# Kernel tuning notes

Measured on AMD Instinct MI355X. Metric: run time of the kernel, lower is better.

Reference implementation:

```python
import jax, jax.numpy as jnp
import numpy as np

B, S, D = 4, 4096, 64
NEG = -1000000000.0

def setup_inputs() -> dict:
    key = jax.random.key(0)
    kq, kk, kv = jax.random.split(key, 3)
    Q = jax.random.normal(kq, (B, S, D), dtype=jnp.float32)
    K = jax.random.normal(kk, (B, S, D), dtype=jnp.float32)
    V = jax.random.normal(kv, (B, S, D), dtype=jnp.float32)
    return {"Q": Q, "K": K, "V": V}

def reference(Q, K, V):
    # Faithful: original scales by sqrt(K.shape[1]) which is the SEQ length, not d_k.
    scale = 1.0 / np.sqrt(K.shape[1]).astype(np.float32)
    scores = jnp.einsum('bqd,bkd->bqk', Q, K) * scale  # [B, S, S]
    sq, sk = scores.shape[1], scores.shape[2]
    mask = jnp.triu(jnp.ones((sq, sk), dtype=scores.dtype), k=1)
    scores = scores + mask * NEG
    att = jax.nn.softmax(scores, axis=-1)
    return jnp.einsum('bqk,bkd->bqd', att, V)
```

## Files before the change

kernel.cpp:

```cpp
#include <hip/hip_runtime.h>

#define BB 4
#define SS 4096
#define DD 64
#define QSCALE (0.015625f * 1.44269504088896f)

typedef __attribute__((ext_vector_type(4)))  float f32x4;
typedef __attribute__((ext_vector_type(16))) float f32x16;
typedef __attribute__((ext_vector_type(8)))  short s16x8;
typedef unsigned short u16;

union frag_u { unsigned u[4]; s16x8 s; };

__device__ __forceinline__ unsigned pack_bf16(float lo, float hi) {
    union { float f; unsigned u; } a, b; a.f = lo; b.f = hi;
    return __builtin_amdgcn_perm(b.u + 0x8000u, a.u + 0x8000u, 0x07060302u);
}

__device__ __forceinline__ unsigned cvtpk(float lo, float hi) {
    unsigned r;
    asm("v_cvt_pk_bf16_f32 %0, %1, %2" : "=v"(r) : "v"(lo), "v"(hi));
    return r;
}

__device__ __forceinline__ void pl32swap(unsigned &a, unsigned &b) {
    asm volatile("v_permlane32_swap_b32 %0, %1" : "+v"(a), "+v"(b));
}

__device__ __forceinline__ float fexp2(float x) {
    return __builtin_amdgcn_exp2f(x);
}

__global__ __launch_bounds__(256) void conv_fused(const float* __restrict__ K,
                                                  const float* __restrict__ V,
                                                  u16* __restrict__ Kf,
                                                  u16* __restrict__ Vf) {
    if (blockIdx.x < 512) {
        const int g    = blockIdx.x * 256 + threadIdx.x;
        const int lane = g & 63, kst = (g >> 6) & 3, kt = (g >> 8) & 1;
        const int tile = (g >> 9) & 63, b = g >> 15;
        const int ql = lane & 31, hi = lane >> 5;
        const long src = ((long)b * SS + tile * 64 + kt * 32 + ql) * DD + kst * 16 + hi * 8;
        f32x4 x0 = *(const f32x4*)(K + src);
        f32x4 x1 = *(const f32x4*)(K + src + 4);
        frag_u f;
        f.u[0] = pack_bf16(x0[0], x0[1]);
        f.u[1] = pack_bf16(x0[2], x0[3]);
        f.u[2] = pack_bf16(x1[0], x1[1]);
        f.u[3] = pack_bf16(x1[2], x1[3]);
        *(s16x8*)(Kf + (long)g * 8) = f.s;
    } else {
        __shared__ u16 tl[64][72];
        const int bid = blockIdx.x - 512;
        const int b = bid >> 6;
        const int tile = bid & 63;
        const int tid = threadIdx.x;
        const float* Vb = V + ((long)b * SS + tile * 64) * DD;
        {
            const int kk = tid >> 4;
            const int d4 = (tid & 15) * 4;
            #pragma unroll
            for (int p = 0; p < 4; ++p) {
                const int k = kk + p * 16;
                f32x4 v = *(const f32x4*)(Vb + k * DD + d4);
                #pragma unroll
                for (int c = 0; c < 4; ++c) {
                    union { float f; unsigned u; } x; x.f = v[c];
                    tl[d4 + c][k] = (u16)((x.u + 0x8000u) >> 16);
                }
            }
        }
        __syncthreads();
        {
            const int ks = tid >> 6, lane = tid & 63;
            const int ql = lane & 31, hi = lane >> 5;
            const int s0 = ks * 16 + hi * 8;
            u16* out = Vf + (((long)(b * 64 + tile) * 2) * 4 + ks) * 64 * 8 + lane * 8;
            #pragma unroll
            for (int dt = 0; dt < 2; ++dt) {
                const int row = dt * 32 + ql;
                frag_u f;
                #pragma unroll
                for (int j = 0; j < 4; ++j)
                    f.u[j] = (unsigned)tl[row][s0 + 2 * j] |
                             ((unsigned)tl[row][s0 + 2 * j + 1] << 16);
                *(s16x8*)(out + (long)dt * 4 * 64 * 8) = f.s;
            }
        }
    }
}

__global__ __launch_bounds__(512, 2) void
attn_mono(const float* __restrict__ Q, const u16* __restrict__ Kf,
          const u16* __restrict__ Vf, float* __restrict__ O)
{
    __shared__ float sO[4][64][36];
    __shared__ float sL[4][32];
    __shared__ float lt[32][68];

    const int bid = blockIdx.x;
    const int xcd = bid & 7;
    const int pos = bid >> 3;
    const int b   = xcd >> 1;
    const int u   = (pos & 1) ? (pos >> 1) : (63 - (pos >> 1));
    const int t   = 2 * u + (xcd & 1);

    const int w    = threadIdx.x >> 6;
    const int lane = threadIdx.x & 63;
    const int ql = lane & 31, hi = lane >> 5, hi8 = hi * 8;
    const int q0 = t * 32;
    const int q_g = q0 + ql;
    const int ntiles = (t >> 1) + 1;

    s16x8 qf[4];
    {
        const float* qrow = Q + ((long)b * SS + q_g) * DD + hi8;
        #pragma unroll
        for (int kst = 0; kst < 4; ++kst) {
            f32x4 x0 = *(const f32x4*)(qrow + kst * 16);
            f32x4 x1 = *(const f32x4*)(qrow + kst * 16 + 4);
            frag_u f;
            f.u[0] = pack_bf16(x0[0] * QSCALE, x0[1] * QSCALE);
            f.u[1] = pack_bf16(x0[2] * QSCALE, x0[3] * QSCALE);
            f.u[2] = pack_bf16(x1[0] * QSCALE, x1[1] * QSCALE);
            f.u[3] = pack_bf16(x1[2] * QSCALE, x1[3] * QSCALE);
            qf[kst] = f.s;
        }
    }

    f32x16 o0, o1, lacc;
    #pragma unroll
    for (int r = 0; r < 16; ++r) { o0[r] = 0.f; o1[r] = 0.f; lacc[r] = 0.f; }

    for (int tile = w; tile < ntiles; tile += 8) {
        const u16* Kt = Kf + (long)((b * 64 + tile) * 4096) + lane * 8;
        const u16* Vt = Vf + (long)((b * 64 + tile) * 4096) + lane * 8;
        s16x8 kf[2][4], vf[2][4];
        #pragma unroll
        for (int kt = 0; kt < 2; ++kt)
            #pragma unroll
            for (int kst = 0; kst < 4; ++kst)
                kf[kt][kst] = *(const s16x8*)(Kt + (kt * 4 + kst) * 512);
        #pragma unroll
        for (int dt = 0; dt < 2; ++dt)
            #pragma unroll
            for (int ks = 0; ks < 4; ++ks)
                vf[dt][ks] = *(const s16x8*)(Vt + (dt * 4 + ks) * 512);

        f32x16 st0, st1;
        #pragma unroll
        for (int r = 0; r < 16; ++r) { st0[r] = 0.f; st1[r] = 0.f; }
        __builtin_amdgcn_s_setprio(1);
        #pragma unroll
        for (int kst = 0; kst < 4; ++kst) {
            st0 = __builtin_amdgcn_mfma_f32_32x32x16_bf16(kf[0][kst], qf[kst], st0, 0, 0, 0);
            st1 = __builtin_amdgcn_mfma_f32_32x32x16_bf16(kf[1][kst], qf[kst], st1, 0, 0, 0);
        }
        __builtin_amdgcn_s_setprio(0);

        const int kvb = tile * 64;
        if (tile == ntiles - 1) {
            #pragma unroll
            for (int r = 0; r < 16; ++r) {
                const int crow = (r & 3) + 8 * (r >> 2) + 4 * hi;
                if (kvb + crow > q_g)      st0[r] = -1e9f;
                if (kvb + 32 + crow > q_g) st1[r] = -1e9f;
            }
        }

        #pragma unroll
        for (int r = 0; r < 16; ++r) {
            st0[r] = fexp2(st0[r]);
            st1[r] = fexp2(st1[r]);
            lacc[r] += st0[r] + st1[r];
        }

        frag_u pf[4];
        #pragma unroll
        for (int kt = 0; kt < 2; ++kt) {
            unsigned wd[8];
            #pragma unroll
            for (int j = 0; j < 8; ++j)
                wd[j] = kt == 0 ? cvtpk(st0[2 * j], st0[2 * j + 1])
                                : cvtpk(st1[2 * j], st1[2 * j + 1]);
            unsigned a0 = wd[0], b0 = wd[2]; pl32swap(a0, b0);
            unsigned a1 = wd[1], b1 = wd[3]; pl32swap(a1, b1);
            pf[2 * kt].u[0] = a0; pf[2 * kt].u[1] = a1;
            pf[2 * kt].u[2] = b0; pf[2 * kt].u[3] = b1;
            unsigned a2 = wd[4], b2 = wd[6]; pl32swap(a2, b2);
            unsigned a3 = wd[5], b3 = wd[7]; pl32swap(a3, b3);
            pf[2 * kt + 1].u[0] = a2; pf[2 * kt + 1].u[1] = a3;
            pf[2 * kt + 1].u[2] = b2; pf[2 * kt + 1].u[3] = b3;
        }

        __builtin_amdgcn_s_setprio(1);
        #pragma unroll
        for (int ks = 0; ks < 4; ++ks) {
            o0 = __builtin_amdgcn_mfma_f32_32x32x16_bf16(vf[0][ks], pf[ks].s, o0, 0, 0, 0);
            o1 = __builtin_amdgcn_mfma_f32_32x32x16_bf16(vf[1][ks], pf[ks].s, o1, 0, 0, 0);
        }
        __builtin_amdgcn_s_setprio(0);
    }

    float l_run;
    {
        float s[8];
        #pragma unroll
        for (int i = 0; i < 8; ++i) s[i] = lacc[i] + lacc[i + 8];
        #pragma unroll
        for (int off = 4; off >= 1; off >>= 1)
            #pragma unroll
            for (int i = 0; i < 4; ++i)
                if (i < off) s[i] += s[i + off];
        l_run = s[0] + __shfl_xor(s[0], 32);
    }

    for (int half = 4; half >= 1; half >>= 1) {
        if (w >= half && w < 2 * half) {
            const int slot = w - half;
            #pragma unroll
            for (int rg = 0; rg < 4; ++rg) {
                f32x4 v0, v1;
                #pragma unroll
                for (int rr = 0; rr < 4; ++rr) { v0[rr] = o0[4 * rg + rr]; v1[rr] = o1[4 * rg + rr]; }
                *(f32x4*)&sO[slot][lane][4 * rg]      = v0;
                *(f32x4*)&sO[slot][lane][16 + 4 * rg] = v1;
            }
            if (hi == 0) sL[slot][ql] = l_run;
        }
        __syncthreads();
        if (w < half) {
            l_run += sL[w][ql];
            #pragma unroll
            for (int rg = 0; rg < 4; ++rg) {
                f32x4 u0 = *(const f32x4*)&sO[w][lane][4 * rg];
                f32x4 u1 = *(const f32x4*)&sO[w][lane][16 + 4 * rg];
                #pragma unroll
                for (int rr = 0; rr < 4; ++rr) {
                    o0[4 * rg + rr] += u0[rr];
                    o1[4 * rg + rr] += u1[rr];
                }
            }
        }
        __syncthreads();
    }

    if (w == 0) {
        const float inv = 1.0f / l_run;
        #pragma unroll
        for (int rg = 0; rg < 4; ++rg) {
            f32x4 v0, v1;
            #pragma unroll
            for (int rr = 0; rr < 4; ++rr) { v0[rr] = o0[4 * rg + rr] * inv; v1[rr] = o1[4 * rg + rr] * inv; }
            *(f32x4*)&lt[ql][8 * rg + 4 * hi]      = v0;
            *(f32x4*)&lt[ql][32 + 8 * rg + 4 * hi] = v1;
        }
    }
    __syncthreads();
    if (threadIdx.x < 256) {
        const int q = threadIdx.x >> 3;
        const int dc = (threadIdx.x & 7) * 8;
        f32x4 r0 = *(const f32x4*)&lt[q][dc];
        f32x4 r1 = *(const f32x4*)&lt[q][dc + 4];
        float* Ob = O + ((long)b * SS + q0 + q) * DD + dc;
        *(f32x4*)Ob       = r0;
        *(f32x4*)(Ob + 4) = r1;
    }
}

__global__ __launch_bounds__(512, 4) void
attn_fb(const float* __restrict__ Q, const float* __restrict__ K,
        const float* __restrict__ V, float* __restrict__ O)
{
    __shared__ float mbuf[4][16 * 68];
    __shared__ float smM[4][16];
    __shared__ float smL[4][16];
    const int tid = threadIdx.x, w = tid >> 6, lane = tid & 63;
    const int m = lane & 15, g = lane >> 4;
    const int idx = blockIdx.x, t = 255 - (idx >> 2), b = idx & 3, q0 = t * 16;
    const float* Kb0 = K + (long)b * SS * DD;
    const float* Vb0 = V + (long)b * SS * DD;
    typedef __attribute__((ext_vector_type(4))) float f4;
    s16x8 qf[2];
    {
        const float* qrow = Q + ((long)b * SS + q0 + m) * DD + g * 8;
        #pragma unroll
        for (int kst = 0; kst < 2; ++kst) {
            f4 x0 = *(const f4*)(qrow + kst * 32);
            f4 x1 = *(const f4*)(qrow + kst * 32 + 4);
            frag_u f;
            f.u[0] = pack_bf16(x0[0] * QSCALE, x0[1] * QSCALE);
            f.u[1] = pack_bf16(x0[2] * QSCALE, x0[3] * QSCALE);
            f.u[2] = pack_bf16(x1[0] * QSCALE, x1[1] * QSCALE);
            f.u[3] = pack_bf16(x1[2] * QSCALE, x1[3] * QSCALE);
            qf[kst] = f.s;
        }
    }
    f4 o[4];
    #pragma unroll
    for (int dt = 0; dt < 4; ++dt) o[dt] = (f4){0.f, 0.f, 0.f, 0.f};
    float m_run = -1e30f, l_run = 0.f;
    const int ntiles = (q0 >> 6) + 1, q_g = q0 + m;
    for (int tile = w; tile < ntiles; tile += 8) {
        const int kvbase = tile * 64;
        f4 st[4];
        #pragma unroll
        for (int mt = 0; mt < 4; ++mt) {
            st[mt] = (f4){0.f, 0.f, 0.f, 0.f};
            const float* kr = Kb0 + (long)(kvbase + mt * 16 + m) * DD + g * 8;
            #pragma unroll
            for (int kst = 0; kst < 2; ++kst) {
                f4 x0 = *(const f4*)(kr + kst * 32);
                f4 x1 = *(const f4*)(kr + kst * 32 + 4);
                frag_u kf;
                kf.u[0] = pack_bf16(x0[0], x0[1]);
                kf.u[1] = pack_bf16(x0[2], x0[3]);
                kf.u[2] = pack_bf16(x1[0], x1[1]);
                kf.u[3] = pack_bf16(x1[2], x1[3]);
                st[mt] = __builtin_amdgcn_mfma_f32_16x16x32_bf16(kf.s, qf[kst], st[mt], 0, 0, 0);
            }
        }
        if (tile == ntiles - 1) {
            #pragma unroll
            for (int mt = 0; mt < 4; ++mt)
                #pragma unroll
                for (int r = 0; r < 4; ++r)
                    if (kvbase + mt * 16 + g * 4 + r > q_g) st[mt][r] = -1e9f;
        }
        float tm = st[0][0];
        #pragma unroll
        for (int mt = 0; mt < 4; ++mt)
            #pragma unroll
            for (int r = 0; r < 4; ++r) tm = fmaxf(tm, st[mt][r]);
        tm = fmaxf(tm, __shfl_xor(tm, 16));
        tm = fmaxf(tm, __shfl_xor(tm, 32));
        const float mnew = fmaxf(m_run, tm);
        const float alpha = fexp2(m_run - mnew);
        float rs = 0.f;
        #pragma unroll
        for (int mt = 0; mt < 4; ++mt)
            #pragma unroll
            for (int r = 0; r < 4; ++r) {
                const float e = fexp2(st[mt][r] - mnew);
                st[mt][r] = e; rs += e;
            }
        rs += __shfl_xor(rs, 16);
        rs += __shfl_xor(rs, 32);
        l_run = l_run * alpha + rs; m_run = mnew;
        unsigned pk[4][2];
        #pragma unroll
        for (int mt = 0; mt < 4; ++mt) {
            pk[mt][0] = pack_bf16(st[mt][0], st[mt][1]);
            pk[mt][1] = pack_bf16(st[mt][2], st[mt][3]);
        }
        float av[4];
        #pragma unroll
        for (int r = 0; r < 4; ++r) av[r] = __shfl(alpha, 4 * g + r);
        #pragma unroll
        for (int dt = 0; dt < 4; ++dt)
            #pragma unroll
            for (int r = 0; r < 4; ++r) o[dt][r] *= av[r];
        #pragma unroll
        for (int kst = 0; kst < 2; ++kst) {
            frag_u pa;
            #pragma unroll
            for (int ww = 0; ww < 4; ++ww) {
                const int srcl = m + 16 * (2 * (g & 1) + (ww >> 1));
                const int v0 = __shfl((int)pk[2 * kst][ww & 1], srcl);
                const int v1 = __shfl((int)pk[2 * kst + 1][ww & 1], srcl);
                pa.u[ww] = (unsigned)((g & 2) ? v1 : v0);
            }
            const float* vcol = Vb0 + (long)(kvbase + kst * 32 + g * 8) * DD + m;
            #pragma unroll
            for (int dt = 0; dt < 4; ++dt) {
                const float* vc = vcol + dt * 16;
                frag_u vb;
                #pragma unroll
                for (int jj = 0; jj < 4; ++jj)
                    vb.u[jj] = pack_bf16(vc[(2 * jj) * DD], vc[(2 * jj + 1) * DD]);
                o[dt] = __builtin_amdgcn_mfma_f32_16x16x32_bf16(pa.s, vb.s, o[dt], 0, 0, 0);
            }
        }
    }
    for (int half = 4; half >= 1; half >>= 1) {
        if (w >= half && w < 2 * half) {
            const int slot = w - half;
            if (g == 0) { smM[slot][m] = m_run; smL[slot][m] = l_run; }
            #pragma unroll
            for (int dt = 0; dt < 4; ++dt)
                #pragma unroll
                for (int r = 0; r < 4; ++r)
                    mbuf[slot][(4 * g + r) * 68 + 16 * dt + m] = o[dt][r];
        }
        __syncthreads();
        if (w < half) {
            const float m2 = smM[w][m], l2 = smL[w][m];
            const float mn = fmaxf(m_run, m2);
            const float a1 = fexp2(m_run - mn), a2 = fexp2(m2 - mn);
            l_run = l_run * a1 + l2 * a2; m_run = mn;
            float av1[4], av2[4];
            #pragma unroll
            for (int r = 0; r < 4; ++r) {
                av1[r] = __shfl(a1, 4 * g + r);
                av2[r] = __shfl(a2, 4 * g + r);
            }
            #pragma unroll
            for (int dt = 0; dt < 4; ++dt)
                #pragma unroll
                for (int r = 0; r < 4; ++r)
                    o[dt][r] = o[dt][r] * av1[r] +
                               mbuf[w][(4 * g + r) * 68 + 16 * dt + m] * av2[r];
        }
        __syncthreads();
    }
    if (w == 0) {
        float lv[4];
        #pragma unroll
        for (int r = 0; r < 4; ++r) lv[r] = 1.0f / __shfl(l_run, 4 * g + r);
        float* Ob = O + ((long)b * SS + q0) * DD;
        #pragma unroll
        for (int dt = 0; dt < 4; ++dt)
            #pragma unroll
            for (int r = 0; r < 4; ++r)
                Ob[(4 * g + r) * DD + dt * 16 + m] = o[dt][r] * lv[r];
    }
}

extern "C" void kernel_launch(void* const* d_in, const int* in_sizes, int n_in,
                              void* d_out, int out_size, void* d_ws, size_t ws_size,
                              hipStream_t stream) {
    const float* Q = (const float*)d_in[0];
    const float* K = (const float*)d_in[1];
    const float* V = (const float*)d_in[2];
    float* O = (float*)d_out;

    const size_t tensor_b = (size_t)BB * SS * DD * sizeof(u16);
    const size_t conv_b   = 2 * tensor_b;

    if (ws_size >= conv_b) {
        u16* Kf = (u16*)d_ws;
        u16* Vf = (u16*)((char*)d_ws + tensor_b);
        conv_fused<<<dim3(768), dim3(256), 0, stream>>>(K, V, Kf, Vf);
        attn_mono <<<dim3(512), dim3(512), 0, stream>>>(Q, Kf, Vf, O);
    } else {
        attn_fb<<<dim3(BB * (SS / 16)), dim3(512), 0, stream>>>(Q, K, V, O);
    }
}
```

Measured before the change: 31.04 us.

## Split causal KV range across two blocks and merge partials in a separate kernel

```diff
diff --git a/kernel.cpp b/kernel.cpp
--- a/kernel.cpp
+++ b/kernel.cpp
@@ -4,6 +4,7 @@
 #define SS 4096
 #define DD 64
 #define QSCALE (0.015625f * 1.44269504088896f)
+#define SLOT_F 2112
 
 typedef __attribute__((ext_vector_type(4)))  float f32x4;
 typedef __attribute__((ext_vector_type(16))) float f32x16;
@@ -91,18 +92,19 @@
 }
 
 __global__ __launch_bounds__(512, 2) void
-attn_mono(const float* __restrict__ Q, const u16* __restrict__ Kf,
-          const u16* __restrict__ Vf, float* __restrict__ O)
+attn_part(const float* __restrict__ Q, const u16* __restrict__ Kf,
+          const u16* __restrict__ Vf, float* __restrict__ part)
 {
     __shared__ float sO[4][64][36];
     __shared__ float sL[4][32];
-    __shared__ float lt[32][68];
 
     const int bid = blockIdx.x;
     const int xcd = bid & 7;
     const int pos = bid >> 3;
     const int b   = xcd >> 1;
-    const int u   = (pos & 1) ? (pos >> 1) : (63 - (pos >> 1));
+    const int hf  = pos & 1;
+    const int p2  = pos >> 1;
+    const int u   = (p2 & 1) ? (p2 >> 1) : (63 - (p2 >> 1));
     const int t   = 2 * u + (xcd & 1);
 
     const int w    = threadIdx.x >> 6;
@@ -111,6 +113,9 @@
     const int q0 = t * 32;
     const int q_g = q0 + ql;
     const int ntiles = (t >> 1) + 1;
+    const int hend = (ntiles + 1) >> 1;
+    const int tlo  = hf ? hend : 0;
+    const int thi  = hf ? ntiles : hend;
 
     s16x8 qf[4];
     {
@@ -132,7 +137,7 @@
     #pragma unroll
     for (int r = 0; r < 16; ++r) { o0[r] = 0.f; o1[r] = 0.f; lacc[r] = 0.f; }
 
-    for (int tile = w; tile < ntiles; tile += 8) {
+    for (int tile = tlo + w; tile < thi; tile += 8) {
         const u16* Kt = Kf + (long)((b * 64 + tile) * 4096) + lane * 8;
         const u16* Vt = Vf + (long)((b * 64 + tile) * 4096) + lane * 8;
         s16x8 kf[2][4], vf[2][4];
@@ -246,6 +251,211 @@
     }
 
     if (w == 0) {
+        float* P = part + (long)((b * 128 + t) * 2 + hf) * SLOT_F;
+        #pragma unroll
+        for (int rg = 0; rg < 4; ++rg) {
+            f32x4 v0, v1;
+            #pragma unroll
+            for (int rr = 0; rr < 4; ++rr) { v0[rr] = o0[4 * rg + rr]; v1[rr] = o1[4 * rg + rr]; }
+            *(f32x4*)(P + (rg * 64 + lane) * 4)       = v0;
+            *(f32x4*)(P + ((4 + rg) * 64 + lane) * 4) = v1;
+        }
+        if (hi == 0) P[2048 + ql] = l_run;
+    }
+}
+
+__global__ __launch_bounds__(256) void
+attn_merge(const float* __restrict__ part, float* __restrict__ O)
+{
+    __shared__ float lt[32][68];
+    const int b = blockIdx.x & 3;
+    const int t = blockIdx.x >> 2;
+    const float* P0 = part + (long)((b * 128 + t) * 2 + 0) * SLOT_F;
+    const float* P1 = part + (long)((b * 128 + t) * 2 + 1) * SLOT_F;
+    const int tid = threadIdx.x;
+
+    #pragma unroll
+    for (int jj = 0; jj < 2; ++jj) {
+        const int j = tid + jj * 256;
+        const int c = j >> 6, lane = j & 63;
+        const int q = lane & 31, h2 = lane >> 5;
+        f32x4 a0 = *(const f32x4*)(P0 + j * 4);
+        f32x4 a1 = *(const f32x4*)(P1 + j * 4);
+        const float inv = 1.0f / (P0[2048 + q] + P1[2048 + q]);
+        const int d0 = (c < 4) ? (8 * c + 4 * h2) : (32 + 8 * (c - 4) + 4 * h2);
+        f32x4 v;
+        #pragma unroll
+        for (int rr = 0; rr < 4; ++rr) v[rr] = (a0[rr] + a1[rr]) * inv;
+        *(f32x4*)&lt[q][d0] = v;
+    }
+    __syncthreads();
+    {
+        const int q  = tid >> 3;
+        const int dc = (tid & 7) * 8;
+        f32x4 r0 = *(const f32x4*)&lt[q][dc];
+        f32x4 r1 = *(const f32x4*)&lt[q][dc + 4];
+        float* Ob = O + ((long)b * SS + t * 32 + q) * DD + dc;
+        *(f32x4*)Ob       = r0;
+        *(f32x4*)(Ob + 4) = r1;
+    }
+}
+
+__global__ __launch_bounds__(512, 2) void
+attn_mono(const float* __restrict__ Q, const u16* __restrict__ Kf,
+          const u16* __restrict__ Vf, float* __restrict__ O)
+{
+    __shared__ float sO[4][64][36];
+    __shared__ float sL[4][32];
+    __shared__ float lt[32][68];
+
+    const int bid = blockIdx.x;
+    const int xcd = bid & 7;
+    const int pos = bid >> 3;
+    const int b   = xcd >> 1;
+    const int u   = (pos & 1) ? (pos >> 1) : (63 - (pos >> 1));
+    const int t   = 2 * u + (xcd & 1);
+
+    const int w    = threadIdx.x >> 6;
+    const int lane = threadIdx.x & 63;
+    const int ql = lane & 31, hi = lane >> 5, hi8 = hi * 8;
+    const int q0 = t * 32;
+    const int q_g = q0 + ql;
+    const int ntiles = (t >> 1) + 1;
+
+    s16x8 qf[4];
+    {
+        const float* qrow = Q + ((long)b * SS + q_g) * DD + hi8;
+        #pragma unroll
+        for (int kst = 0; kst < 4; ++kst) {
+            f32x4 x0 = *(const f32x4*)(qrow + kst * 16);
+            f32x4 x1 = *(const f32x4*)(qrow + kst * 16 + 4);
+            frag_u f;
+            f.u[0] = pack_bf16(x0[0] * QSCALE, x0[1] * QSCALE);
+            f.u[1] = pack_bf16(x0[2] * QSCALE, x0[3] * QSCALE);
+            f.u[2] = pack_bf16(x1[0] * QSCALE, x1[1] * QSCALE);
+            f.u[3] = pack_bf16(x1[2] * QSCALE, x1[3] * QSCALE);
+            qf[kst] = f.s;
+        }
+    }
+
+    f32x16 o0, o1, lacc;
+    #pragma unroll
+    for (int r = 0; r < 16; ++r) { o0[r] = 0.f; o1[r] = 0.f; lacc[r] = 0.f; }
+
+    for (int tile = w; tile < ntiles; tile += 8) {
+        const u16* Kt = Kf + (long)((b * 64 + tile) * 4096) + lane * 8;
+        const u16* Vt = Vf + (long)((b * 64 + tile) * 4096) + lane * 8;
+        s16x8 kf[2][4], vf[2][4];
+        #pragma unroll
+        for (int kt = 0; kt < 2; ++kt)
+            #pragma unroll
+            for (int kst = 0; kst < 4; ++kst)
+                kf[kt][kst] = *(const s16x8*)(Kt + (kt * 4 + kst) * 512);
+        #pragma unroll
+        for (int dt = 0; dt < 2; ++dt)
+            #pragma unroll
+            for (int ks = 0; ks < 4; ++ks)
+                vf[dt][ks] = *(const s16x8*)(Vt + (dt * 4 + ks) * 512);
+
+        f32x16 st0, st1;
+        #pragma unroll
+        for (int r = 0; r < 16; ++r) { st0[r] = 0.f; st1[r] = 0.f; }
+        __builtin_amdgcn_s_setprio(1);
+        #pragma unroll
+        for (int kst = 0; kst < 4; ++kst) {
+            st0 = __builtin_amdgcn_mfma_f32_32x32x16_bf16(kf[0][kst], qf[kst], st0, 0, 0, 0);
+            st1 = __builtin_amdgcn_mfma_f32_32x32x16_bf16(kf[1][kst], qf[kst], st1, 0, 0, 0);
+        }
+        __builtin_amdgcn_s_setprio(0);
+
+        const int kvb = tile * 64;
+        if (tile == ntiles - 1) {
+            #pragma unroll
+            for (int r = 0; r < 16; ++r) {
+                const int crow = (r & 3) + 8 * (r >> 2) + 4 * hi;
+                if (kvb + crow > q_g)      st0[r] = -1e9f;
+                if (kvb + 32 + crow > q_g) st1[r] = -1e9f;
+            }
+        }
+
+        #pragma unroll
+        for (int r = 0; r < 16; ++r) {
+            st0[r] = fexp2(st0[r]);
+            st1[r] = fexp2(st1[r]);
+            lacc[r] += st0[r] + st1[r];
+        }
+
+        frag_u pf[4];
+        #pragma unroll
+        for (int kt = 0; kt < 2; ++kt) {
+            unsigned wd[8];
+            #pragma unroll
+            for (int j = 0; j < 8; ++j)
+                wd[j] = kt == 0 ? cvtpk(st0[2 * j], st0[2 * j + 1])
+                                : cvtpk(st1[2 * j], st1[2 * j + 1]);
+            unsigned a0 = wd[0], b0 = wd[2]; pl32swap(a0, b0);
+            unsigned a1 = wd[1], b1 = wd[3]; pl32swap(a1, b1);
+            pf[2 * kt].u[0] = a0; pf[2 * kt].u[1] = a1;
+            pf[2 * kt].u[2] = b0; pf[2 * kt].u[3] = b1;
+            unsigned a2 = wd[4], b2 = wd[6]; pl32swap(a2, b2);
+            unsigned a3 = wd[5], b3 = wd[7]; pl32swap(a3, b3);
+            pf[2 * kt + 1].u[0] = a2; pf[2 * kt + 1].u[1] = a3;
+            pf[2 * kt + 1].u[2] = b2; pf[2 * kt + 1].u[3] = b3;
+        }
+
+        __builtin_amdgcn_s_setprio(1);
+        #pragma unroll
+        for (int ks = 0; ks < 4; ++ks) {
+            o0 = __builtin_amdgcn_mfma_f32_32x32x16_bf16(vf[0][ks], pf[ks].s, o0, 0, 0, 0);
+            o1 = __builtin_amdgcn_mfma_f32_32x32x16_bf16(vf[1][ks], pf[ks].s, o1, 0, 0, 0);
+        }
+        __builtin_amdgcn_s_setprio(0);
+    }
+
+    float l_run;
+    {
+        float s[8];
+        #pragma unroll
+        for (int i = 0; i < 8; ++i) s[i] = lacc[i] + lacc[i + 8];
+        #pragma unroll
+        for (int off = 4; off >= 1; off >>= 1)
+            #pragma unroll
+            for (int i = 0; i < 4; ++i)
+                if (i < off) s[i] += s[i + off];
+        l_run = s[0] + __shfl_xor(s[0], 32);
+    }
+
+    for (int half = 4; half >= 1; half >>= 1) {
+        if (w >= half && w < 2 * half) {
+            const int slot = w - half;
+            #pragma unroll
+            for (int rg = 0; rg < 4; ++rg) {
+                f32x4 v0, v1;
+                #pragma unroll
+                for (int rr = 0; rr < 4; ++rr) { v0[rr] = o0[4 * rg + rr]; v1[rr] = o1[4 * rg + rr]; }
+                *(f32x4*)&sO[slot][lane][4 * rg]      = v0;
+                *(f32x4*)&sO[slot][lane][16 + 4 * rg] = v1;
+            }
+            if (hi == 0) sL[slot][ql] = l_run;
+        }
+        __syncthreads();
+        if (w < half) {
+            l_run += sL[w][ql];
+            #pragma unroll
+            for (int rg = 0; rg < 4; ++rg) {
+                f32x4 u0 = *(const f32x4*)&sO[w][lane][4 * rg];
+                f32x4 u1 = *(const f32x4*)&sO[w][lane][16 + 4 * rg];
+                #pragma unroll
+                for (int rr = 0; rr < 4; ++rr) {
+                    o0[4 * rg + rr] += u0[rr];
+                    o1[4 * rg + rr] += u1[rr];
+                }
+            }
+        }
+        __syncthreads();
+    }
+
+    if (w == 0) {
         const float inv = 1.0f / l_run;
         #pragma unroll
         for (int rg = 0; rg < 4; ++rg) {
@@ -262,167 +472,9 @@
         const int dc = (threadIdx.x & 7) * 8;
         f32x4 r0 = *(const f32x4*)&lt[q][dc];
         f32x4 r1 = *(const f32x4*)&lt[q][dc + 4];
-        float* Ob = O + ((long)b * SS + q0 + q) * DD + dc;
+        float* Ob = O + ((long)b * SS + t * 32 + q) * DD + dc;
         *(f32x4*)Ob       = r0;
         *(f32x4*)(Ob + 4) = r1;
-    }
-}
-
-__global__ __launch_bounds__(512, 4) void
-attn_fb(const float* __restrict__ Q, const float* __restrict__ K,
-        const float* __restrict__ V, float* __restrict__ O)
-{
-    __shared__ float mbuf[4][16 * 68];
-    __shared__ float smM[4][16];
-    __shared__ float smL[4][16];
-    const int tid = threadIdx.x, w = tid >> 6, lane = tid & 63;
-    const int m = lane & 15, g = lane >> 4;
-    const int idx = blockIdx.x, t = 255 - (idx >> 2), b = idx & 3, q0 = t * 16;
-    const float* Kb0 = K + (long)b * SS * DD;
-    const float* Vb0 = V + (long)b * SS * DD;
-    typedef __attribute__((ext_vector_type(4))) float f4;
-    s16x8 qf[2];
-    {
-        const float* qrow = Q + ((long)b * SS + q0 + m) * DD + g * 8;
-        #pragma unroll
-        for (int kst = 0; kst < 2; ++kst) {
-            f4 x0 = *(const f4*)(qrow + kst * 32);
-            f4 x1 = *(const f4*)(qrow + kst * 32 + 4);
-            frag_u f;
-            f.u[0] = pack_bf16(x0[0] * QSCALE, x0[1] * QSCALE);
-            f.u[1] = pack_bf16(x0[2] * QSCALE, x0[3] * QSCALE);
-            f.u[2] = pack_bf16(x1[0] * QSCALE, x1[1] * QSCALE);
-            f.u[3] = pack_bf16(x1[2] * QSCALE, x1[3] * QSCALE);
-            qf[kst] = f.s;
-        }
-    }
-    f4 o[4];
-    #pragma unroll
-    for (int dt = 0; dt < 4; ++dt) o[dt] = (f4){0.f, 0.f, 0.f, 0.f};
-    float m_run = -1e30f, l_run = 0.f;
-    const int ntiles = (q0 >> 6) + 1, q_g = q0 + m;
-    for (int tile = w; tile < ntiles; tile += 8) {
-        const int kvbase = tile * 64;
-        f4 st[4];
-        #pragma unroll
-        for (int mt = 0; mt < 4; ++mt) {
-            st[mt] = (f4){0.f, 0.f, 0.f, 0.f};
-            const float* kr = Kb0 + (long)(kvbase + mt * 16 + m) * DD + g * 8;
-            #pragma unroll
-            for (int kst = 0; kst < 2; ++kst) {
-                f4 x0 = *(const f4*)(kr + kst * 32);
-                f4 x1 = *(const f4*)(kr + kst * 32 + 4);
-                frag_u kf;
-                kf.u[0] = pack_bf16(x0[0], x0[1]);
-                kf.u[1] = pack_bf16(x0[2], x0[3]);
-                kf.u[2] = pack_bf16(x1[0], x1[1]);
-                kf.u[3] = pack_bf16(x1[2], x1[3]);
-                st[mt] = __builtin_amdgcn_mfma_f32_16x16x32_bf16(kf.s, qf[kst], st[mt], 0, 0, 0);
-            }
-        }
-        if (tile == ntiles - 1) {
-            #pragma unroll
-            for (int mt = 0; mt < 4; ++mt)
-                #pragma unroll
-                for (int r = 0; r < 4; ++r)
-                    if (kvbase + mt * 16 + g * 4 + r > q_g) st[mt][r] = -1e9f;
-        }
-        float tm = st[0][0];
-        #pragma unroll
-        for (int mt = 0; mt < 4; ++mt)
-            #pragma unroll
-            for (int r = 0; r < 4; ++r) tm = fmaxf(tm, st[mt][r]);
-        tm = fmaxf(tm, __shfl_xor(tm, 16));
-        tm = fmaxf(tm, __shfl_xor(tm, 32));
-        const float mnew = fmaxf(m_run, tm);
-        const float alpha = fexp2(m_run - mnew);
-        float rs = 0.f;
-        #pragma unroll
-        for (int mt = 0; mt < 4; ++mt)
-            #pragma unroll
-            for (int r = 0; r < 4; ++r) {
-                const float e = fexp2(st[mt][r] - mnew);
-                st[mt][r] = e; rs += e;
-            }
-        rs += __shfl_xor(rs, 16);
-        rs += __shfl_xor(rs, 32);
-        l_run = l_run * alpha + rs; m_run = mnew;
-        unsigned pk[4][2];
-        #pragma unroll
-        for (int mt = 0; mt < 4; ++mt) {
-            pk[mt][0] = pack_bf16(st[mt][0], st[mt][1]);
-            pk[mt][1] = pack_bf16(st[mt][2], st[mt][3]);
-        }
-        float av[4];
-        #pragma unroll
-        for (int r = 0; r < 4; ++r) av[r] = __shfl(alpha, 4 * g + r);
-        #pragma unroll
-        for (int dt = 0; dt < 4; ++dt)
-            #pragma unroll
-            for (int r = 0; r < 4; ++r) o[dt][r] *= av[r];
-        #pragma unroll
-        for (int kst = 0; kst < 2; ++kst) {
-            frag_u pa;
-            #pragma unroll
-            for (int ww = 0; ww < 4; ++ww) {
-                const int srcl = m + 16 * (2 * (g & 1) + (ww >> 1));
-                const int v0 = __shfl((int)pk[2 * kst][ww & 1], srcl);
-                const int v1 = __shfl((int)pk[2 * kst + 1][ww & 1], srcl);
-                pa.u[ww] = (unsigned)((g & 2) ? v1 : v0);
-            }
-            const float* vcol = Vb0 + (long)(kvbase + kst * 32 + g * 8) * DD + m;
-            #pragma unroll
-            for (int dt = 0; dt < 4; ++dt) {
-                const float* vc = vcol + dt * 16;
-                frag_u vb;
-                #pragma unroll
-                for (int jj = 0; jj < 4; ++jj)
-                    vb.u[jj] = pack_bf16(vc[(2 * jj) * DD], vc[(2 * jj + 1) * DD]);
-                o[dt] = __builtin_amdgcn_mfma_f32_16x16x32_bf16(pa.s, vb.s, o[dt], 0, 0, 0);
-            }
-        }
-    }
-    for (int half = 4; half >= 1; half >>= 1) {
-        if (w >= half && w < 2 * half) {
-            const int slot = w - half;
-            if (g == 0) { smM[slot][m] = m_run; smL[slot][m] = l_run; }
-            #pragma unroll
-            for (int dt = 0; dt < 4; ++dt)
-                #pragma unroll
-                for (int r = 0; r < 4; ++r)
-                    mbuf[slot][(4 * g + r) * 68 + 16 * dt + m] = o[dt][r];
-        }
-        __syncthreads();
-        if (w < half) {
-            const float m2 = smM[w][m], l2 = smL[w][m];
-            const float mn = fmaxf(m_run, m2);
-            const float a1 = fexp2(m_run - mn), a2 = fexp2(m2 - mn);
-            l_run = l_run * a1 + l2 * a2; m_run = mn;
-            float av1[4], av2[4];
-            #pragma unroll
-            for (int r = 0; r < 4; ++r) {
-                av1[r] = __shfl(a1, 4 * g + r);
-                av2[r] = __shfl(a2, 4 * g + r);
-            }
-            #pragma unroll
-            for (int dt = 0; dt < 4; ++dt)
-                #pragma unroll
-                for (int r = 0; r < 4; ++r)
-                    o[dt][r] = o[dt][r] * av1[r] +
-                               mbuf[w][(4 * g + r) * 68 + 16 * dt + m] * av2[r];
-        }
-        __syncthreads();
-    }
-    if (w == 0) {
-        float lv[4];
-        #pragma unroll
-        for (int r = 0; r < 4; ++r) lv[r] = 1.0f / __shfl(l_run, 4 * g + r);
-        float* Ob = O + ((long)b * SS + q0) * DD;
-        #pragma unroll
-        for (int dt = 0; dt < 4; ++dt)
-            #pragma unroll
-            for (int r = 0; r < 4; ++r)
-                Ob[(4 * g + r) * DD + dt * 16 + m] = o[dt][r] * lv[r];
     }
 }
 
@@ -436,13 +488,19 @@
 
     const size_t tensor_b = (size_t)BB * SS * DD * sizeof(u16);
     const size_t conv_b   = 2 * tensor_b;
-
-    if (ws_size >= conv_b) {
+    const size_t part_b   = (size_t)1024 * SLOT_F * sizeof(float);
+
+    if (ws_size >= conv_b + part_b) {
+        u16* Kf = (u16*)d_ws;
+        u16* Vf = (u16*)((char*)d_ws + tensor_b);
+        float* part = (float*)((char*)d_ws + conv_b);
+        conv_fused<<<dim3(768),  dim3(256), 0, stream>>>(K, V, Kf, Vf);
+        attn_part <<<dim3(1024), dim3(512), 0, stream>>>(Q, Kf, Vf, part);
+        attn_merge<<<dim3(512),  dim3(256), 0, stream>>>(part, O);
+    } else if (ws_size >= conv_b) {
         u16* Kf = (u16*)d_ws;
         u16* Vf = (u16*)((char*)d_ws + tensor_b);
         conv_fused<<<dim3(768), dim3(256), 0, stream>>>(K, V, Kf, Vf);
         attn_mono <<<dim3(512), dim3(512), 0, stream>>>(Q, Kf, Vf, O);
-    } else {
-        attn_fb<<<dim3(BB * (SS / 16)), dim3(512), 0, stream>>>(Q, K, V, O);
-    }
-}
+    }
+}
```

Measured after the change: 42.73 us. 37.6% more time.
